# Optimization experiments

Hardware: AMD Instinct MI355X
Metric: run time of the kernel (lower is better)

## Reference

```python
import jax, jax.numpy as jnp
import numpy as np

B, N, F_IN, H, OUT = 64, 1024, 195, 128, 64
K1, K2 = N // 2, N // 4  # ceil(0.5*N), ceil(0.5*K1)
EPS = 1e-5


def setup_inputs() -> dict:
    key = jax.random.key(0)
    ks = jax.random.split(key, 16)
    rn = lambda k, s: jax.random.normal(k, s, dtype=jnp.float32) * 0.1
    inp = {
        "input": jax.random.normal(ks[0], (B, N, F_IN), dtype=jnp.float32),
        # SAGEConv1 (195->128): lin_l (neighbors, w/ bias), lin_r (root, no bias)
        "W1l": rn(ks[1], (H, F_IN)), "b1l": jnp.zeros((H,), jnp.float32),
        "W1r": rn(ks[2], (H, F_IN)),
        # SAGPooling1 GNN = GraphConv(128->1): lin_rel (sum aggr, w/ bias), lin_root (no bias)
        "Wp1_rel": rn(ks[3], (1, H)), "bp1_rel": jnp.zeros((1,), jnp.float32),
        "Wp1_root": rn(ks[4], (1, H)),
        # SAGEConv2 (128->64)
        "W2l": rn(ks[5], (OUT, H)), "b2l": jnp.zeros((OUT,), jnp.float32),
        "W2r": rn(ks[6], (OUT, H)),
        # SAGPooling2 GNN = GraphConv(64->1)
        "Wp2_rel": rn(ks[7], (1, OUT)), "bp2_rel": jnp.zeros((1,), jnp.float32),
        "Wp2_root": rn(ks[8], (1, OUT)),
        # MLP head
        "fc1_w": rn(ks[9], (512, OUT)), "fc1_b": jnp.zeros((512,), jnp.float32),
        "bn1_g": jnp.ones((512,), jnp.float32), "bn1_b": jnp.zeros((512,), jnp.float32),
        "bn1_m": jnp.zeros((512,), jnp.float32), "bn1_v": jnp.ones((512,), jnp.float32),
        "fc2_w": rn(ks[10], (256, 512)), "fc2_b": jnp.zeros((256,), jnp.float32),
        "bn2_g": jnp.ones((256,), jnp.float32), "bn2_b": jnp.zeros((256,), jnp.float32),
        "bn2_m": jnp.zeros((256,), jnp.float32), "bn2_v": jnp.ones((256,), jnp.float32),
        "fc3_w": rn(ks[11], (2, 256)), "fc3_b": jnp.zeros((2,), jnp.float32),
    }
    return inp


def _corr_adj(x):
    # Pearson corrcoef over rows of x [B,N,F] -> boolean adjacency [B,N,N] (corr > 0.5)
    xc = x - x.mean(axis=-1, keepdims=True)
    cov = jnp.einsum("bnf,bmf->bnm", xc, xc)
    d = jnp.sqrt(jnp.clip(jnp.einsum("bnnf->bn", cov[..., None] * 0 + 0) + jnp.diagonal(cov, axis1=1, axis2=2), 1e-12))
    corr = cov / (d[:, :, None] * d[:, None, :])
    return (corr > 0.5).astype(x.dtype)  # symmetric, includes self-loops


def _sage(x, A, Wl, bl, Wr):
    # PyG SAGEConv: lin_l(mean_{j in N(i)} x_j) + lin_r(x_i)
    deg = A.sum(axis=-1, keepdims=True)
    agg = jnp.einsum("bnm,bmf->bnf", A, x) / jnp.maximum(deg, 1.0)
    return jnp.einsum("bnf,hf->bnh", agg, Wl) + bl + jnp.einsum("bnf,hf->bnh", x, Wr)


def _sagpool(x, A, Wrel, brel, Wroot, k):
    # score via GraphConv (sum aggr): lin_rel(sum_j x_j) + lin_root(x_i)
    agg = jnp.einsum("bnm,bmf->bnf", A, x)
    score = (jnp.einsum("bnf,of->bno", agg, Wrel) + brel
             + jnp.einsum("bnf,of->bno", x, Wroot))[..., 0]  # [B,N]
    top_s, idx = jax.lax.top_k(score, k)  # per-graph top-k nodes
    x_new = jnp.take_along_axis(x, idx[:, :, None], axis=1) * jnp.tanh(top_s)[:, :, None]
    A_new = jnp.take_along_axis(A, idx[:, :, None], axis=1)
    A_new = jnp.take_along_axis(A_new, idx[:, None, :], axis=2)
    return x_new, A_new


def _bn_eval(x, g, b, m, v):
    return g * (x - m) * jax.lax.rsqrt(v + EPS) + b


def reference(input, W1l, b1l, W1r, Wp1_rel, bp1_rel, Wp1_root,
              W2l, b2l, W2r, Wp2_rel, bp2_rel, Wp2_root,
              fc1_w, fc1_b, bn1_g, bn1_b, bn1_m, bn1_v,
              fc2_w, fc2_b, bn2_g, bn2_b, bn2_m, bn2_v,
              fc3_w, fc3_b):
    A = _corr_adj(input)                                   # [B,N,N]
    x = jax.nn.relu(_sage(input, A, W1l, b1l, W1r))        # [B,N,128]
    x, A = _sagpool(x, A, Wp1_rel, bp1_rel, Wp1_root, K1)  # [B,K1,128]
    x = jax.nn.relu(_sage(x, A, W2l, b2l, W2r))            # [B,K1,64]
    x, A = _sagpool(x, A, Wp2_rel, bp2_rel, Wp2_root, K2)  # [B,K2,64]
    x = x.mean(axis=1)                                     # global mean pool -> [B,64]
    x = _bn_eval(jax.nn.relu(x @ fc1_w.T + fc1_b), bn1_g, bn1_b, bn1_m, bn1_v)
    x = _bn_eval(jax.nn.relu(x @ fc2_w.T + fc2_b), bn2_g, bn2_b, bn2_m, bn2_v)
    x = x @ fc3_w.T + fc3_b
    return jax.nn.softmax(x, axis=1)
```

## Files before the change

### kernel.cpp

```cpp
#include <hip/hip_runtime.h>
#include <hip/hip_fp8.h>
#include <cstdint>


typedef __bf16 bf16x8 __attribute__((ext_vector_type(8)));
typedef float  floatx4 __attribute__((ext_vector_type(4)));

#define MFMA_BF16(a, b, c) __builtin_amdgcn_mfma_f32_16x16x32_bf16((a), (b), (c), 0, 0, 0)
#define MFMA_FP8(a, b, c)  __builtin_amdgcn_mfma_f32_16x16x32_fp8_fp8((a), (b), (c), 0, 0, 0)

typedef __attribute__((address_space(1))) const void as1_cvoid;
typedef __attribute__((address_space(3))) void as3_void;
static __device__ __forceinline__ void gl16(const void* g, void* l) {
  __builtin_amdgcn_global_load_lds((as1_cvoid*)g, (as3_void*)l, 16, 0, 0);
}

static constexpr int BATCH = 64, NNODE = 1024, FIN = 195, FPAD = 224;
static constexpr int HD = 128, OD = 64, KP1 = 512, KP2 = 256;

static constexpr size_t OFF_GHI   = 0;
static constexpr size_t OFF_GLO   = 8388608;
static constexpr size_t OFF_A1B   = 16777216;
static constexpr size_t OFF_YR2   = 18874368;
static constexpr size_t OFF_X2    = 35651584;
static constexpr size_t OFF_XHI   = 0;
static constexpr size_t OFF_XLO   = 29360128;
static constexpr size_t OFF_ABITS = 58720256;
static constexpr size_t OFF_X1    = 67108864;
static constexpr size_t OFF_P1    = 100663296;
static constexpr size_t OFF_Q1    = OFF_P1 + 262144;
static constexpr size_t OFF_IDX1  = OFF_Q1 + 262144;
static constexpr size_t OFF_GATE1 = OFF_IDX1 + 131072;
static constexpr size_t OFF_P2    = OFF_GATE1 + 131072;
static constexpr size_t OFF_Q2    = OFF_P2 + 131072;
static constexpr size_t OFF_W1HI  = OFF_Q2 + 131072;
static constexpr size_t OFF_W1LO  = OFF_W1HI + 114688;
static constexpr size_t OFF_W2HI  = OFF_W1LO + 114688;
static constexpr size_t OFF_W2LO  = OFF_W2HI + 32768;
static constexpr size_t OFF_XHAT  = 102760448;
static constexpr size_t OFF_YR1   = 102760448 + 16777216;

static __device__ __forceinline__ unsigned char to_fp8(float v) {
  __hip_fp8_e4m3 q(v);
  return *(unsigned char*)&q;
}

__global__ __launch_bounds__(256) void prep_pack_kernel(
    const float* __restrict__ x, __bf16* __restrict__ xhi,
    __bf16* __restrict__ xlo, unsigned char* __restrict__ xhat8,
    const float* __restrict__ W1l, const float* __restrict__ W1r,
    __bf16* __restrict__ hi1, __bf16* __restrict__ lo1,
    const float* __restrict__ W2l, const float* __restrict__ W2r,
    __bf16* __restrict__ hi2, __bf16* __restrict__ lo2) {
  int bid = blockIdx.x;
  if (bid < 16384) {
    int row  = bid * 4 + (threadIdx.x >> 6);
    int lane = threadIdx.x & 63;
    const float* xr = x + (long)row * FIN;
    int k0 = lane * 4;
    float v[4];
#pragma unroll
    for (int i = 0; i < 4; ++i) v[i] = (k0 + i < FIN) ? xr[k0 + i] : 0.f;
    float s = v[0] + v[1] + v[2] + v[3];
#pragma unroll
    for (int o = 32; o; o >>= 1) s += __shfl_xor(s, o);
    float mean = s * (1.f / (float)FIN);
    float c[4], ss = 0.f;
#pragma unroll
    for (int i = 0; i < 4; ++i) {
      c[i] = (k0 + i < FIN) ? (v[i] - mean) : 0.f;
      ss += c[i] * c[i];
    }
#pragma unroll
    for (int o = 32; o; o >>= 1) ss += __shfl_xor(ss, o);
    float inv = rsqrtf(fmaxf(ss, 1e-12f));
    if (k0 < FPAD) {
      __bf16 hi4[4], lo4[4];
      unsigned char h8[4];
#pragma unroll
      for (int i = 0; i < 4; ++i) {
        float xv = (k0 + i < FIN) ? v[i] : 0.f;
        __bf16 h = (__bf16)xv;
        hi4[i] = h;
        lo4[i] = (__bf16)(xv - (float)h);
        h8[i] = to_fp8(c[i] * inv);
      }
      long base = (long)row * FPAD + k0;
      *(uint2*)&xhi[base] = *(const uint2*)hi4;
      *(uint2*)&xlo[base] = *(const uint2*)lo4;
      *(unsigned int*)&xhat8[base] = *(const unsigned int*)h8;
    }
  } else if (bid < 16384 + 224) {
    int idx = (bid - 16384) * 256 + threadIdx.x;
    int h = idx / FPAD, k = idx % FPAD;
    float v = 0.f;
    if (k < FIN) v = (h < HD) ? W1l[h * FIN + k] : W1r[(h - HD) * FIN + k];
    __bf16 a = (__bf16)v;
    hi1[idx] = a;
    lo1[idx] = (__bf16)(v - (float)a);
  } else {
    int idx = (bid - 16384 - 224) * 256 + threadIdx.x;
    int h = idx / HD, k = idx % HD;
    float v = (h < OD) ? W2l[h * HD + k] : W2r[(h - OD) * HD + k];
    __bf16 a = (__bf16)v;
    hi2[idx] = a;
    lo2[idx] = (__bf16)(v - (float)a);
  }
}

static constexpr int CKB = 48;
__global__ __launch_bounds__(256) void corr_kernel(
    const unsigned char* __restrict__ xhat8, unsigned short* __restrict__ Abits) {
  __shared__ __align__(16) unsigned char sI[128 * CKB];
  __shared__ __align__(16) unsigned char sJ[128 * CKB];
  int bid = blockIdx.x;
  int xcd = bid & 7;
  int m = bid >> 3;
  int b = xcd + ((m & 7) << 3);
  int rem = m >> 3, bi = 0;
  while (rem >= 8 - bi) { rem -= 8 - bi; ++bi; }
  int bj = bi + rem;
  int i0 = bi * 128, j0 = bj * 128;
  const unsigned char* Xb = xhat8 + (long)b * NNODE * FPAD;
  int lane = threadIdx.x & 63, wave = threadIdx.x >> 6;
  int wi = (wave >> 1) * 64, wj = (wave & 1) * 64;
  int lr = lane & 15, lk8 = (lane >> 4) * 8;
  int strow = threadIdx.x & 127;
  int sbuf = threadIdx.x >> 7;
  floatx4 zero = {0.f, 0.f, 0.f, 0.f};
  floatx4 acc[4][4];
#pragma unroll
  for (int i = 0; i < 4; ++i)
#pragma unroll
    for (int j = 0; j < 4; ++j) acc[i][j] = zero;
  for (int kk = 0; kk < 7; ++kk) {
    int k0 = kk * 32;
    __syncthreads();
    {
      unsigned char* dst = (sbuf ? sJ : sI) + strow * CKB;
      const unsigned char* src = Xb + (long)((sbuf ? j0 : i0) + strow) * FPAD + k0;
      *(uint4*)(dst)      = *(const uint4*)(src);
      *(uint4*)(dst + 16) = *(const uint4*)(src + 16);
    }
    __syncthreads();
    long long af[4], bf[4];
#pragma unroll
    for (int t = 0; t < 4; ++t) {
      af[t] = *(const long long*)&sI[(wi + t * 16 + lr) * CKB + lk8];
      bf[t] = *(const long long*)&sJ[(wj + t * 16 + lr) * CKB + lk8];
    }
#pragma unroll
    for (int ti = 0; ti < 4; ++ti)
#pragma unroll
      for (int tj = 0; tj < 4; ++tj)
        acc[ti][tj] = MFMA_FP8(af[ti], bf[tj], acc[ti][tj]);
  }
#pragma unroll
  for (int ti = 0; ti < 4; ++ti)
#pragma unroll
    for (int tj = 0; tj < 4; ++tj) {
      floatx4 a = acc[ti][tj];
      unsigned long long m0 = __ballot(a[0] > 0.5f);
      unsigned long long m1 = __ballot(a[1] > 0.5f);
      unsigned long long m2 = __ballot(a[2] > 0.5f);
      unsigned long long m3 = __ballot(a[3] > 0.5f);
      if (lane < 16) {
        unsigned long long mm = (lane & 2) ? ((lane & 1) ? m3 : m2)
                                           : ((lane & 1) ? m1 : m0);
        unsigned short piece = (unsigned short)(mm >> ((lane >> 2) * 16));
        int grow = i0 + wi + ti * 16 + lane;
        int gcol = (j0 + wj + tj * 16) >> 4;
        Abits[((long)b * NNODE + grow) * 64 + gcol] = piece;
      }
    }
}

template <int K, int NCOL>
__global__ __launch_bounds__(256, 3) void gemm_split_kernel(
    const __bf16* __restrict__ Ahi, const __bf16* __restrict__ Alo,
    const __bf16* __restrict__ Bhi, const __bf16* __restrict__ Blo,
    float* __restrict__ C, int mblocks,
    unsigned long long* __restrict__ A64, int ntrans) {
  constexpr int ldc = NCOL * 128;
  int bid = blockIdx.x;
  if (bid >= mblocks * NCOL) {
    int t = bid - mblocks * NCOL;
    if (t >= ntrans) return;
    int b = t / 28, pi = t % 28;
    int rem = pi, rb = 1;
    while (rem >= rb) { rem -= rb; ++rb; }
    int cb = rem;
    int wave = threadIdx.x >> 6, lane = threadIdx.x & 63;
    int dr = rb * 2 + (wave >> 1);
    int dc = cb * 2 + (wave & 1);
    long base = (long)b * NNODE;
    unsigned long long xv = A64[(base + dc * 64 + lane) * 16 + dr];
    const unsigned long long M1  = 0x5555555555555555ULL;
    const unsigned long long M2  = 0x3333333333333333ULL;
    const unsigned long long M4  = 0x0F0F0F0F0F0F0F0FULL;
    const unsigned long long M8  = 0x00FF00FF00FF00FFULL;
    const unsigned long long M16 = 0x0000FFFF0000FFFFULL;
    const unsigned long long M32 = 0x00000000FFFFFFFFULL;
#define TSTEP(Kk, M)                                                      \
    {                                                                     \
      unsigned long long y = __shfl_xor(xv, Kk);                          \
      xv = ((lane & Kk) == 0) ? ((xv & (M)) | ((y & (M)) << Kk))          \
                              : ((xv & ~(M)) | ((y & ~(M)) >> Kk));       \
    }
    TSTEP(1, M1) TSTEP(2, M2) TSTEP(4, M4) TSTEP(8, M8) TSTEP(16, M16) TSTEP(32, M32)
#undef TSTEP
    A64[(base + dr * 64 + lane) * 16 + dc] = xv;
    return;
  }
  int mrow, col;
  if (NCOL == 2) {
    int xcd = bid & 7;
    int q = bid >> 3;
    col = q & 1;
    mrow = (xcd << 6) + (q >> 1);
  } else {
    mrow = bid;
    col = 0;
  }
  __shared__ __align__(16) __bf16 sAh[128 * 32];
  __shared__ __align__(16) __bf16 sAl[128 * 32];
  __shared__ __align__(16) __bf16 sBh[128 * 32];
  __shared__ __align__(16) __bf16 sBl[128 * 32];
  long row0 = (long)mrow * 128;
  int col0 = col * 128;
  int t = threadIdx.x;
  int lane = t & 63, wave = t >> 6;
  int wi = (wave >> 1) * 64, wj = (wave & 1) * 64;
  int lr = lane & 15, lk2 = (lane >> 4) * 16;
  int sr = t >> 2, sc = (t & 3) * 8;
  const char* gA0 = (const char*)(Ahi + (row0 + sr) * (long)K + sc);
  const char* gA1 = (const char*)(Alo + (row0 + sr) * (long)K + sc);
  const char* gB0 = (const char*)(Bhi + (long)(col0 + sr) * K + sc);
  const char* gB1 = (const char*)(Blo + (long)(col0 + sr) * K + sc);
  constexpr long rstep = 64L * K * 2;
  char* lAh = (char*)sAh + (wave << 10);
  char* lAl = (char*)sAl + (wave << 10);
  char* lBh = (char*)sBh + (wave << 10);
  char* lBl = (char*)sBl + (wave << 10);
  floatx4 zero = {0.f, 0.f, 0.f, 0.f};
  floatx4 acc[4][4];
#pragma unroll
  for (int i = 0; i < 4; ++i)
#pragma unroll
    for (int j = 0; j < 4; ++j) acc[i][j] = zero;
  for (int kk = 0; kk < (K >> 5); ++kk) {
    __syncthreads();
    gl16(gA0, lAh); gl16(gA0 + rstep, lAh + 4096);
    gl16(gA1, lAl); gl16(gA1 + rstep, lAl + 4096);
    gl16(gB0, lBh); gl16(gB0 + rstep, lBh + 4096);
    gl16(gB1, lBl); gl16(gB1 + rstep, lBl + 4096);
    gA0 += 64; gA1 += 64; gB0 += 64; gB1 += 64;
    __syncthreads();
    bf16x8 bh[4], bl[4];
#pragma unroll
    for (int tj = 0; tj < 4; ++tj) {
      bh[tj] = *(const bf16x8*)((const char*)sBh + (wj + tj * 16 + lr) * 64 + lk2);
      bl[tj] = *(const bf16x8*)((const char*)sBl + (wj + tj * 16 + lr) * 64 + lk2);
    }
#pragma unroll
    for (int ti = 0; ti < 4; ++ti) {
      bf16x8 ah = *(const bf16x8*)((const char*)sAh + (wi + ti * 16 + lr) * 64 + lk2);
      bf16x8 al = *(const bf16x8*)((const char*)sAl + (wi + ti * 16 + lr) * 64 + lk2);
#pragma unroll
      for (int tj = 0; tj < 4; ++tj) acc[ti][tj] = MFMA_BF16(ah, bh[tj], acc[ti][tj]);
#pragma unroll
      for (int tj = 0; tj < 4; ++tj) acc[ti][tj] = MFMA_BF16(ah, bl[tj], acc[ti][tj]);
#pragma unroll
      for (int tj = 0; tj < 4; ++tj) acc[ti][tj] = MFMA_BF16(al, bh[tj], acc[ti][tj]);
    }
  }
#pragma unroll
  for (int ti = 0; ti < 4; ++ti)
#pragma unroll
    for (int tj = 0; tj < 4; ++tj)
#pragma unroll
      for (int rr = 0; rr < 4; ++rr) {
        long grow = row0 + wi + ti * 16 + (lane >> 4) * 4 + rr;
        int gcol = col0 + wj + tj * 16 + (lane & 15);
        C[grow * ldc + gcol] = acc[ti][tj][rr];
      }
}

__global__ __launch_bounds__(256) void sage1_kernel(
    const unsigned int* __restrict__ Abits32, const float* __restrict__ YR1,
    const float* __restrict__ b1l, const float* __restrict__ Wrel,
    const float* __restrict__ Wroot, float* __restrict__ x1,
    float* __restrict__ p1, float* __restrict__ q1) {
  int g = threadIdx.x >> 5;
  int lane = threadIdx.x & 31;
  int node = blockIdx.x * 8 + g;
  int b = node >> 10, nloc = node & 1023;
  __shared__ int list[8][1024];
  __shared__ int s_deg[8];
  {
    unsigned int word = Abits32[(long)node * 32 + lane];
    int cnt = __popc(word);
    int off = cnt;
#pragma unroll
    for (int o = 1; o < 32; o <<= 1) {
      int v = __shfl_up(off, o, 32);
      if (lane >= o) off += v;
    }
    off -= cnt;
    if (lane == 31) s_deg[g] = off + cnt;
    int basei = lane * 32;
    while (word) {
      int t = __ffs(word) - 1;
      word &= word - 1;
      list[g][off++] = basei + t;
    }
  }
  __syncthreads();
  int deg = s_deg[g];
  const float4* Y4 = (const float4*)(YR1 + (long)(b << 10) * 256);
  float4 a4 = {0.f, 0.f, 0.f, 0.f};
  for (int d = 0; d < deg; ++d) {
    float4 y = Y4[(long)list[g][d] * 64 + lane];
    a4.x += y.x; a4.y += y.y; a4.z += y.z; a4.w += y.w;
  }
  float4 R = Y4[(long)nloc * 64 + 32 + lane];
  float inv = 1.f / (float)(deg < 1 ? 1 : deg);
  float4 bl = ((const float4*)b1l)[lane];
  float4 v;
  v.x = fmaxf(a4.x * inv + bl.x + R.x, 0.f);
  v.y = fmaxf(a4.y * inv + bl.y + R.y, 0.f);
  v.z = fmaxf(a4.z * inv + bl.z + R.z, 0.f);
  v.w = fmaxf(a4.w * inv + bl.w + R.w, 0.f);
  ((float4*)x1)[(long)node * 32 + lane] = v;
  float4 wr = ((const float4*)Wrel)[lane];
  float4 wq = ((const float4*)Wroot)[lane];
  float pv = v.x * wr.x + v.y * wr.y + v.z * wr.z + v.w * wr.w;
  float qv = v.x * wq.x + v.y * wq.y + v.z * wq.z + v.w * wq.w;
#pragma unroll
  for (int o = 16; o; o >>= 1) {
    pv += __shfl_xor(pv, o, 32);
    qv += __shfl_xor(qv, o, 32);
  }
  if (lane == 0) { p1[node] = pv; q1[node] = qv; }
}

__global__ void scoretopk_kernel(const unsigned int* __restrict__ bits32,
                                 const float* __restrict__ p,
                                 const float* __restrict__ q,
                                 const float* __restrict__ brel,
                                 int* __restrict__ idx_out,
                                 float* __restrict__ gate_out,
                                 int nwords, int rpb_shift, int k) {
  int b = blockIdx.x, tid = threadIdx.x;
  int row = (b << rpb_shift) + tid;
  const unsigned int* wptr = bits32 + (long)row * nwords;
  const float* pb = p + ((long)b << rpb_shift);
  float s = q[row] + brel[0];
  for (int w = 0; w < nwords; ++w) {
    unsigned int word = wptr[w];
    while (word) {
      int t = __ffs(word) - 1;
      word &= word - 1;
      s += pb[w * 32 + t];
    }
  }
  unsigned int fb = __float_as_uint(s);
  unsigned int key = (fb & 0x80000000u) ? ~fb : (fb | 0x80000000u);
  __shared__ int hist[256];
  __shared__ unsigned int sh_prefix;
  __shared__ int sh_target, cnt_gt, cnt_eq, outpos;
  if (tid == 0) { sh_prefix = 0; sh_target = k; cnt_gt = 0; cnt_eq = 0; outpos = 0; }
  for (int shift = 24; shift >= 0; shift -= 8) {
    if (tid < 256) hist[tid] = 0;
    __syncthreads();
    unsigned int prefix = sh_prefix;
    bool inset = (shift == 24) || ((key >> (shift + 8)) == (prefix >> (shift + 8)));
    if (inset) atomicAdd(&hist[(key >> shift) & 255], 1);
    __syncthreads();
    if (tid < 64) {
      int lane = tid;
      int bb0 = hist[255 - 4 * lane];
      int bb1 = hist[254 - 4 * lane];
      int bb2 = hist[253 - 4 * lane];
      int bb3 = hist[252 - 4 * lane];
      int c0 = bb0, c1 = c0 + bb1, c2 = c1 + bb2, c3 = c2 + bb3;
      int incl = c3;
#pragma unroll
      for (int o = 1; o < 64; o <<= 1) {
        int v = __shfl_up(incl, o);
        if (lane >= o) incl += v;
      }
      int excl = incl - c3;
      int target = sh_target;
      int cum[4] = {excl + c0, excl + c1, excl + c2, excl + c3};
      int prev = excl;
#pragma unroll
      for (int i = 0; i < 4; ++i) {
        if (cum[i] >= target && prev < target) {
          int bin = 255 - (4 * lane + i);
          sh_prefix = prefix | ((unsigned int)bin << shift);
          sh_target = target - prev;
        }
        prev = cum[i];
      }
    }
    __syncthreads();
  }
  unsigned int T = sh_prefix;
  if (key > T) atomicAdd(&cnt_gt, 1);
  __syncthreads();
  int E = k - cnt_gt;
  bool sel = (key > T);
  if (!sel && key == T) sel = (atomicAdd(&cnt_eq, 1) < E);
  if (sel) {
    int posn = atomicAdd(&outpos, 1);
    idx_out[b * k + posn] = tid;
    gate_out[b * k + posn] = tanhf(s);
  }
}

__global__ __launch_bounds__(256) void gather_kernel(
    const float* __restrict__ x1, const int* __restrict__ idx,
    const float* __restrict__ gate, __bf16* __restrict__ ghi,
    __bf16* __restrict__ glo, const unsigned int* __restrict__ Abits32,
    unsigned long long* __restrict__ A1bits) {
  int bid = blockIdx.x;
  if (bid < 16384) {
    long e = (long)bid * 256 + threadIdx.x;
    int h = (int)(e & 127);
    int i = (int)((e >> 7) & 511);
    int b = (int)(e >> 16);
    int srow = idx[(b << 9) + i];
    float v = x1[((long)(b << 10) + srow) * 128 + h] * gate[(b << 9) + i];
    __bf16 a = (__bf16)v;
    ghi[e] = a;
    glo[e] = (__bf16)(v - (float)a);
  } else {
    int gi = (bid - 16384) * 4 + (threadIdx.x >> 6);
    int lane = threadIdx.x & 63;
    int b = gi >> 9;
    int srow = idx[gi];
    const unsigned int* src = Abits32 + ((long)(b << 10) + srow) * 32;
    const int* idxb = idx + (b << 9);
#pragma unroll
    for (int t = 0; t < 8; ++t) {
      int cj = idxb[t * 64 + lane];
      int bit = (src[cj >> 5] >> (cj & 31)) & 1;
      unsigned long long m = __ballot(bit);
      if (lane == 0) A1bits[(long)gi * 8 + t] = m;
    }
  }
}

__global__ __launch_bounds__(256) void sage2_kernel(
    const unsigned int* __restrict__ A1b32, const float* __restrict__ YR2,
    const float* __restrict__ b2l, const float* __restrict__ Wrel,
    const float* __restrict__ Wroot, float* __restrict__ x2,
    float* __restrict__ p2, float* __restrict__ q2) {
  int g = threadIdx.x >> 4;
  int lane = threadIdx.x & 15;
  int row = blockIdx.x * 16 + g;
  int b = row >> 9, iloc = row & 511;
  __shared__ int list[16][512];
  __shared__ int s_deg[16];
  {
    unsigned int word = A1b32[(long)row * 16 + lane];
    int cnt = __popc(word);
    int off = cnt;
#pragma unroll
    for (int o = 1; o < 16; o <<= 1) {
      int v = __shfl_up(off, o, 16);
      if (lane >= o) off += v;
    }
    off -= cnt;
    if (lane == 15) s_deg[g] = off + cnt;
    int basei = lane * 32;
    while (word) {
      int t = __ffs(word) - 1;
      word &= word - 1;
      list[g][off++] = basei + t;
    }
  }
  __syncthreads();
  int deg = s_deg[g];
  const float4* Y4 = (const float4*)(YR2 + (long)(b << 9) * 128);
  float4 a4 = {0.f, 0.f, 0.f, 0.f};
  for (int d = 0; d < deg; ++d) {
    float4 y = Y4[(long)list[g][d] * 32 + lane];
    a4.x += y.x; a4.y += y.y; a4.z += y.z; a4.w += y.w;
  }
  float4 R = Y4[(long)iloc * 32 + 16 + lane];
  float inv = 1.f / (float)(deg < 1 ? 1 : deg);
  float4 bl = ((const float4*)b2l)[lane];
  float4 v;
  v.x = fmaxf(a4.x * inv + bl.x + R.x, 0.f);
  v.y = fmaxf(a4.y * inv + bl.y + R.y, 0.f);
  v.z = fmaxf(a4.z * inv + bl.z + R.z, 0.f);
  v.w = fmaxf(a4.w * inv + bl.w + R.w, 0.f);
  ((float4*)x2)[(long)row * 16 + lane] = v;
  float4 wr = ((const float4*)Wrel)[lane];
  float4 wq = ((const float4*)Wroot)[lane];
  float pv = v.x * wr.x + v.y * wr.y + v.z * wr.z + v.w * wr.w;
  float qv = v.x * wq.x + v.y * wq.y + v.z * wq.z + v.w * wq.w;
#pragma unroll
  for (int o = 8; o; o >>= 1) {
    pv += __shfl_xor(pv, o, 16);
    qv += __shfl_xor(qv, o, 16);
  }
  if (lane == 0) { p2[row] = pv; q2[row] = qv; }
}

__global__ __launch_bounds__(512) void scoretopk_head_kernel(
    const unsigned int* __restrict__ A1b32, const float* __restrict__ p2,
    const float* __restrict__ q2, const float* __restrict__ brel,
    const float* __restrict__ x2, const float* __restrict__ fc1_w,
    const float* __restrict__ fc1_b, const float* __restrict__ g1,
    const float* __restrict__ bb1, const float* __restrict__ m1,
    const float* __restrict__ v1, const float* __restrict__ fc2_w,
    const float* __restrict__ fc2_b, const float* __restrict__ g2,
    const float* __restrict__ bb2, const float* __restrict__ m2,
    const float* __restrict__ v2, const float* __restrict__ fc3_w,
    const float* __restrict__ fc3_b, float* __restrict__ out) {
  int b = blockIdx.x, tid = threadIdx.x;
  int row = (b << 9) + tid;
  const unsigned int* wptr = A1b32 + (long)row * 16;
  const float* pb = p2 + ((long)b << 9);
  float s = q2[row] + brel[0];
  for (int w = 0; w < 16; ++w) {
    unsigned int word = wptr[w];
    while (word) {
      int t = __ffs(word) - 1;
      word &= word - 1;
      s += pb[w * 32 + t];
    }
  }
  constexpr int k = KP2;
  unsigned int fb = __float_as_uint(s);
  unsigned int key = (fb & 0x80000000u) ? ~fb : (fb | 0x80000000u);
  __shared__ int hist[256];
  __shared__ int idx2s[256];
  __shared__ float gate2s[256];
  __shared__ unsigned int sh_prefix;
  __shared__ int sh_target, cnt_gt, cnt_eq, outpos;
  if (tid == 0) { sh_prefix = 0; sh_target = k; cnt_gt = 0; cnt_eq = 0; outpos = 0; }
  for (int shift = 24; shift >= 0; shift -= 8) {
    if (tid < 256) hist[tid] = 0;
    __syncthreads();
    unsigned int prefix = sh_prefix;
    bool inset = (shift == 24) || ((key >> (shift + 8)) == (prefix >> (shift + 8)));
    if (inset) atomicAdd(&hist[(key >> shift) & 255], 1);
    __syncthreads();
    if (tid < 64) {
      int lane = tid;
      int bb0 = hist[255 - 4 * lane];
      int bb1 = hist[254 - 4 * lane];
      int bb2 = hist[253 - 4 * lane];
      int bb3 = hist[252 - 4 * lane];
      int c0 = bb0, c1 = c0 + bb1, c2 = c1 + bb2, c3 = c2 + bb3;
      int incl = c3;
#pragma unroll
      for (int o = 1; o < 64; o <<= 1) {
        int v = __shfl_up(incl, o);
        if (lane >= o) incl += v;
      }
      int excl = incl - c3;
      int target = sh_target;
      int cum[4] = {excl + c0, excl + c1, excl + c2, excl + c3};
      int prev = excl;
#pragma unroll
      for (int i = 0; i < 4; ++i) {
        if (cum[i] >= target && prev < target) {
          int bin = 255 - (4 * lane + i);
          sh_prefix = prefix | ((unsigned int)bin << shift);
          sh_target = target - prev;
        }
        prev = cum[i];
      }
    }
    __syncthreads();
  }
  unsigned int T = sh_prefix;
  if (key > T) atomicAdd(&cnt_gt, 1);
  __syncthreads();
  int E = k - cnt_gt;
  bool sel = (key > T);
  if (!sel && key == T) sel = (atomicAdd(&cnt_eq, 1) < E);
  if (sel) {
    int posn = atomicAdd(&outpos, 1);
    idx2s[posn] = tid;
    gate2s[posn] = tanhf(s);
  }
  __syncthreads();
  __shared__ float part[8][64];
  __shared__ float pooled[64];
  __shared__ float h1[512];
  __shared__ float h2[256];
  __shared__ float zz[2];
  int h = tid & 63, grp = tid >> 6;
  float sp = 0.f;
  for (int i = grp * 32; i < grp * 32 + 32; ++i) {
    int si = idx2s[i];
    sp += x2[((long)(b << 9) + si) * 64 + h] * gate2s[i];
  }
  part[grp][h] = sp;
  __syncthreads();
  if (tid < 64) {
    float t = 0.f;
#pragma unroll
    for (int g = 0; g < 8; ++g) t += part[g][tid];
    pooled[tid] = t * (1.f / 256.f);
  }
  __syncthreads();
  {
    float z = fc1_b[tid];
    for (int j = 0; j < 64; ++j) z += pooled[j] * fc1_w[tid * 64 + j];
    z = fmaxf(z, 0.f);
    h1[tid] = g1[tid] * (z - m1[tid]) * rsqrtf(v1[tid] + 1e-5f) + bb1[tid];
  }
  __syncthreads();
  if (tid < 256) {
    float z = fc2_b[tid];
    for (int j = 0; j < 512; ++j) z += h1[j] * fc2_w[tid * 512 + j];
    z = fmaxf(z, 0.f);
    h2[tid] = g2[tid] * (z - m2[tid]) * rsqrtf(v2[tid] + 1e-5f) + bb2[tid];
  }
  __syncthreads();
  if (tid < 2) {
    float z = fc3_b[tid];
    for (int j = 0; j < 256; ++j) z += h2[j] * fc3_w[tid * 256 + j];
    zz[tid] = z;
  }
  __syncthreads();
  if (tid == 0) {
    float mx = fmaxf(zz[0], zz[1]);
    float e0 = expf(zz[0] - mx), e1 = expf(zz[1] - mx);
    float inv = 1.f / (e0 + e1);
    out[b * 2 + 0] = e0 * inv;
    out[b * 2 + 1] = e1 * inv;
  }
}

extern "C" void kernel_launch(void* const* d_in, const int* in_sizes, int n_in,
                              void* d_out, int out_size, void* d_ws, size_t ws_size,
                              hipStream_t stream) {
  (void)in_sizes; (void)n_in; (void)out_size; (void)ws_size;
  const float* input   = (const float*)d_in[0];
  const float* W1l     = (const float*)d_in[1];
  const float* b1l     = (const float*)d_in[2];
  const float* W1r     = (const float*)d_in[3];
  const float* Wp1_rel = (const float*)d_in[4];
  const float* bp1_rel = (const float*)d_in[5];
  const float* Wp1_root= (const float*)d_in[6];
  const float* W2l     = (const float*)d_in[7];
  const float* b2l     = (const float*)d_in[8];
  const float* W2r     = (const float*)d_in[9];
  const float* Wp2_rel = (const float*)d_in[10];
  const float* bp2_rel = (const float*)d_in[11];
  const float* Wp2_root= (const float*)d_in[12];
  const float* fc1_w   = (const float*)d_in[13];
  const float* fc1_b   = (const float*)d_in[14];
  const float* bn1_g   = (const float*)d_in[15];
  const float* bn1_b   = (const float*)d_in[16];
  const float* bn1_m   = (const float*)d_in[17];
  const float* bn1_v   = (const float*)d_in[18];
  const float* fc2_w   = (const float*)d_in[19];
  const float* fc2_b   = (const float*)d_in[20];
  const float* bn2_g   = (const float*)d_in[21];
  const float* bn2_b   = (const float*)d_in[22];
  const float* bn2_m   = (const float*)d_in[23];
  const float* bn2_v   = (const float*)d_in[24];
  const float* fc3_w   = (const float*)d_in[25];
  const float* fc3_b   = (const float*)d_in[26];

  char* ws = (char*)d_ws;
  __bf16* xhi   = (__bf16*)(ws + OFF_XHI);
  __bf16* xlo   = (__bf16*)(ws + OFF_XLO);
  unsigned char* xhat8 = (unsigned char*)(ws + OFF_XHAT);
  unsigned short* Abits = (unsigned short*)(ws + OFF_ABITS);
  const unsigned int* Abits32 = (const unsigned int*)(ws + OFF_ABITS);
  unsigned long long* A64 = (unsigned long long*)(ws + OFF_ABITS);
  float* YR1    = (float*)(ws + OFF_YR1);
  float* x1     = (float*)(ws + OFF_X1);
  float* p1     = (float*)(ws + OFF_P1);
  float* q1     = (float*)(ws + OFF_Q1);
  int*   idx1   = (int*)(ws + OFF_IDX1);
  float* gate1  = (float*)(ws + OFF_GATE1);
  float* p2     = (float*)(ws + OFF_P2);
  float* q2     = (float*)(ws + OFF_Q2);
  __bf16* w1hi  = (__bf16*)(ws + OFF_W1HI);
  __bf16* w1lo  = (__bf16*)(ws + OFF_W1LO);
  __bf16* w2hi  = (__bf16*)(ws + OFF_W2HI);
  __bf16* w2lo  = (__bf16*)(ws + OFF_W2LO);
  __bf16* ghi   = (__bf16*)(ws + OFF_GHI);
  __bf16* glo   = (__bf16*)(ws + OFF_GLO);
  unsigned long long* A1bits = (unsigned long long*)(ws + OFF_A1B);
  const unsigned int* A1b32  = (const unsigned int*)(ws + OFF_A1B);
  float* YR2    = (float*)(ws + OFF_YR2);
  float* x2     = (float*)(ws + OFF_X2);
  float* out    = (float*)d_out;

  prep_pack_kernel<<<16672, 256, 0, stream>>>(input, xhi, xlo, xhat8,
                                              W1l, W1r, w1hi, w1lo,
                                              W2l, W2r, w2hi, w2lo);
  corr_kernel<<<2304, 256, 0, stream>>>(xhat8, Abits);
  gemm_split_kernel<224, 2><<<1024 + 1792, 256, 0, stream>>>(
      xhi, xlo, w1hi, w1lo, YR1, 512, A64, 1792);
  sage1_kernel<<<8192, 256, 0, stream>>>(Abits32, YR1, b1l, Wp1_rel, Wp1_root, x1, p1, q1);
  scoretopk_kernel<<<64, 1024, 0, stream>>>(Abits32, p1, q1, bp1_rel, idx1, gate1,
                                            32, 10, KP1);
  gather_kernel<<<24576, 256, 0, stream>>>(x1, idx1, gate1, ghi, glo, Abits32, A1bits);
  gemm_split_kernel<128, 1><<<256, 256, 0, stream>>>(
      ghi, glo, w2hi, w2lo, YR2, 256, nullptr, 0);
  sage2_kernel<<<2048, 256, 0, stream>>>(A1b32, YR2, b2l, Wp2_rel, Wp2_root, x2, p2, q2);
  scoretopk_head_kernel<<<64, 512, 0, stream>>>(A1b32, p2, q2, bp2_rel, x2,
                                                fc1_w, fc1_b, bn1_g, bn1_b, bn1_m, bn1_v,
                                                fc2_w, fc2_b, bn2_g, bn2_b, bn2_m, bn2_v,
                                                fc3_w, fc3_b, out);
}
```

Baseline: 337.8 us.

## Double-buffer split-bf16 GEMM LDS with swizzle; warp-reduce MLP head matvecs

```diff
diff --git a/kernel.cpp b/kernel.cpp
--- a/kernel.cpp
+++ b/kernel.cpp
@@ -176,7 +176,7 @@
 }
 
 template <int K, int NCOL>
-__global__ __launch_bounds__(256, 3) void gemm_split_kernel(
+__global__ __launch_bounds__(256, 2) void gemm_split_kernel(
     const __bf16* __restrict__ Ahi, const __bf16* __restrict__ Alo,
     const __bf16* __restrict__ Bhi, const __bf16* __restrict__ Blo,
     float* __restrict__ C, int mblocks,
@@ -222,50 +222,61 @@
     mrow = bid;
     col = 0;
   }
-  __shared__ __align__(16) __bf16 sAh[128 * 32];
-  __shared__ __align__(16) __bf16 sAl[128 * 32];
-  __shared__ __align__(16) __bf16 sBh[128 * 32];
-  __shared__ __align__(16) __bf16 sBl[128 * 32];
+  __shared__ __align__(16) __bf16 sAh[2][4096];
+  __shared__ __align__(16) __bf16 sAl[2][4096];
+  __shared__ __align__(16) __bf16 sBh[2][4096];
+  __shared__ __align__(16) __bf16 sBl[2][4096];
   long row0 = (long)mrow * 128;
   int col0 = col * 128;
   int t = threadIdx.x;
   int lane = t & 63, wave = t >> 6;
   int wi = (wave >> 1) * 64, wj = (wave & 1) * 64;
   int lr = lane & 15, lk2 = (lane >> 4) * 16;
-  int sr = t >> 2, sc = (t & 3) * 8;
-  const char* gA0 = (const char*)(Ahi + (row0 + sr) * (long)K + sc);
-  const char* gA1 = (const char*)(Alo + (row0 + sr) * (long)K + sc);
-  const char* gB0 = (const char*)(Bhi + (long)(col0 + sr) * K + sc);
-  const char* gB1 = (const char*)(Blo + (long)(col0 + sr) * K + sc);
+  int lk2s = lk2 ^ (((lr >> 1) & 3) << 4);
+  int sr = t >> 2;
+  int scb = (((t & 3) ^ ((sr >> 1) & 3)) << 4);
+  const char* gA0 = (const char*)Ahi + (row0 + sr) * (long)K * 2 + scb;
+  const char* gA1 = (const char*)Alo + (row0 + sr) * (long)K * 2 + scb;
+  const char* gB0 = (const char*)Bhi + (long)(col0 + sr) * K * 2 + scb;
+  const char* gB1 = (const char*)Blo + (long)(col0 + sr) * K * 2 + scb;
   constexpr long rstep = 64L * K * 2;
-  char* lAh = (char*)sAh + (wave << 10);
-  char* lAl = (char*)sAl + (wave << 10);
-  char* lBh = (char*)sBh + (wave << 10);
-  char* lBl = (char*)sBl + (wave << 10);
+  int woff = wave << 10;
+  auto stage = [&](int buf, int kc) {
+    long ko = (long)kc * 64;
+    char* dAh = (char*)&sAh[buf][0] + woff;
+    char* dAl = (char*)&sAl[buf][0] + woff;
+    char* dBh = (char*)&sBh[buf][0] + woff;
+    char* dBl = (char*)&sBl[buf][0] + woff;
+    gl16(gA0 + ko, dAh); gl16(gA0 + ko + rstep, dAh + 4096);
+    gl16(gA1 + ko, dAl); gl16(gA1 + ko + rstep, dAl + 4096);
+    gl16(gB0 + ko, dBh); gl16(gB0 + ko + rstep, dBh + 4096);
+    gl16(gB1 + ko, dBl); gl16(gB1 + ko + rstep, dBl + 4096);
+  };
   floatx4 zero = {0.f, 0.f, 0.f, 0.f};
   floatx4 acc[4][4];
 #pragma unroll
   for (int i = 0; i < 4; ++i)
 #pragma unroll
     for (int j = 0; j < 4; ++j) acc[i][j] = zero;
+  stage(0, 0);
+  __syncthreads();
+  int cur = 0;
   for (int kk = 0; kk < (K >> 5); ++kk) {
-    __syncthreads();
-    gl16(gA0, lAh); gl16(gA0 + rstep, lAh + 4096);
-    gl16(gA1, lAl); gl16(gA1 + rstep, lAl + 4096);
-    gl16(gB0, lBh); gl16(gB0 + rstep, lBh + 4096);
-    gl16(gB1, lBl); gl16(gB1 + rstep, lBl + 4096);
-    gA0 += 64; gA1 += 64; gB0 += 64; gB1 += 64;
-    __syncthreads();
+    if (kk + 1 < (K >> 5)) stage(cur ^ 1, kk + 1);
+    const char* rAh = (const char*)&sAh[cur][0];
+    const char* rAl = (const char*)&sAl[cur][0];
+    const char* rBh = (const char*)&sBh[cur][0];
+    const char* rBl = (const char*)&sBl[cur][0];
     bf16x8 bh[4], bl[4];
 #pragma unroll
     for (int tj = 0; tj < 4; ++tj) {
-      bh[tj] = *(const bf16x8*)((const char*)sBh + (wj + tj * 16 + lr) * 64 + lk2);
-      bl[tj] = *(const bf16x8*)((const char*)sBl + (wj + tj * 16 + lr) * 64 + lk2);
+      bh[tj] = *(const bf16x8*)(rBh + (wj + tj * 16 + lr) * 64 + lk2s);
+      bl[tj] = *(const bf16x8*)(rBl + (wj + tj * 16 + lr) * 64 + lk2s);
     }
 #pragma unroll
     for (int ti = 0; ti < 4; ++ti) {
-      bf16x8 ah = *(const bf16x8*)((const char*)sAh + (wi + ti * 16 + lr) * 64 + lk2);
-      bf16x8 al = *(const bf16x8*)((const char*)sAl + (wi + ti * 16 + lr) * 64 + lk2);
+      bf16x8 ah = *(const bf16x8*)(rAh + (wi + ti * 16 + lr) * 64 + lk2s);
+      bf16x8 al = *(const bf16x8*)(rAl + (wi + ti * 16 + lr) * 64 + lk2s);
 #pragma unroll
       for (int tj = 0; tj < 4; ++tj) acc[ti][tj] = MFMA_BF16(ah, bh[tj], acc[ti][tj]);
 #pragma unroll
@@ -273,6 +284,8 @@
 #pragma unroll
       for (int tj = 0; tj < 4; ++tj) acc[ti][tj] = MFMA_BF16(al, bh[tj], acc[ti][tj]);
     }
+    __syncthreads();
+    cur ^= 1;
   }
 #pragma unroll
   for (int ti = 0; ti < 4; ++ti)
@@ -592,9 +605,9 @@
   }
   __syncthreads();
   __shared__ float part[8][64];
-  __shared__ float pooled[64];
-  __shared__ float h1[512];
-  __shared__ float h2[256];
+  __shared__ __align__(16) float pooled[64];
+  __shared__ __align__(16) float h1[512];
+  __shared__ __align__(16) float h2[256];
   __shared__ float zz[2];
   int h = tid & 63, grp = tid >> 6;
   float sp = 0.f;
@@ -611,24 +624,52 @@
     pooled[tid] = t * (1.f / 256.f);
   }
   __syncthreads();
+  int lane = tid & 63, wv = tid >> 6;
   {
-    float z = fc1_b[tid];
-    for (int j = 0; j < 64; ++j) z += pooled[j] * fc1_w[tid * 64 + j];
-    z = fmaxf(z, 0.f);
+    float pl = pooled[lane];
+#pragma unroll 4
+    for (int i = 0; i < 64; ++i) {
+      int o = wv * 64 + i;
+      float z = pl * fc1_w[o * 64 + lane];
+#pragma unroll
+      for (int off = 32; off; off >>= 1) z += __shfl_xor(z, off);
+      if (lane == 0) h1[o] = z;
+    }
+  }
+  __syncthreads();
+  {
+    float z = fmaxf(h1[tid] + fc1_b[tid], 0.f);
     h1[tid] = g1[tid] * (z - m1[tid]) * rsqrtf(v1[tid] + 1e-5f) + bb1[tid];
   }
   __syncthreads();
+  {
+    float4 hA = *(const float4*)&h1[lane * 8];
+    float4 hB = *(const float4*)&h1[lane * 8 + 4];
+#pragma unroll 4
+    for (int i = 0; i < 32; ++i) {
+      int o = wv * 32 + i;
+      const float4* wr = (const float4*)&fc2_w[o * 512 + lane * 8];
+      float4 w0 = wr[0], w1 = wr[1];
+      float z = hA.x * w0.x + hA.y * w0.y + hA.z * w0.z + hA.w * w0.w
+              + hB.x * w1.x + hB.y * w1.y + hB.z * w1.z + hB.w * w1.w;
+#pragma unroll
+      for (int off = 32; off; off >>= 1) z += __shfl_xor(z, off);
+      if (lane == 0) h2[o] = z;
+    }
+  }
+  __syncthreads();
   if (tid < 256) {
-    float z = fc2_b[tid];
-    for (int j = 0; j < 512; ++j) z += h1[j] * fc2_w[tid * 512 + j];
-    z = fmaxf(z, 0.f);
+    float z = fmaxf(h2[tid] + fc2_b[tid], 0.f);
     h2[tid] = g2[tid] * (z - m2[tid]) * rsqrtf(v2[tid] + 1e-5f) + bb2[tid];
   }
   __syncthreads();
-  if (tid < 2) {
-    float z = fc3_b[tid];
-    for (int j = 0; j < 256; ++j) z += h2[j] * fc3_w[tid * 256 + j];
-    zz[tid] = z;
+  if (wv < 2) {
+    float4 hv = *(const float4*)&h2[lane * 4];
+    float4 wv4 = *(const float4*)&fc3_w[wv * 256 + lane * 4];
+    float z = hv.x * wv4.x + hv.y * wv4.y + hv.z * wv4.z + hv.w * wv4.w;
+#pragma unroll
+    for (int off = 32; off; off >>= 1) z += __shfl_xor(z, off);
+    if (lane == 0) zz[wv] = z + fc3_b[wv];
   }
   __syncthreads();
   if (tid == 0) {
```

Result: slower. 369.9 us (+9.5%).
